# Optimization experiments

Measured on AMD Instinct MI355X. Metric: run time of the kernel, lower is better.

Reference implementation:

```python
import jax, jax.numpy as jnp
import numpy as np

D_MODEL = 512
N_EXPERTS = 8


def setup_inputs() -> dict:
    key = jax.random.key(0)
    ks = jax.random.split(key, 7)
    B, S, D, E = 8, 2048, D_MODEL, N_EXPERTS
    scale = 1.0 / np.sqrt(D)
    x = jax.random.normal(ks[0], (B, S, D), dtype=jnp.float32)
    W1 = jax.random.normal(ks[1], (E, D, D), dtype=jnp.float32) * scale
    b1 = jax.random.normal(ks[2], (E, D), dtype=jnp.float32) * scale
    W2 = jax.random.normal(ks[3], (E, D, D), dtype=jnp.float32) * scale
    b2 = jax.random.normal(ks[4], (E, D), dtype=jnp.float32) * scale
    Wg = jax.random.normal(ks[5], (D, E), dtype=jnp.float32) * scale
    bg = jax.random.normal(ks[6], (E,), dtype=jnp.float32) * scale
    return {"x": x, "W1": W1, "b1": b1, "W2": W2, "b2": b2, "Wg": Wg, "bg": bg}


def reference(x, W1, b1, W2, b2, Wg, bg):
    # All-experts dense MLP: h[e,b,s,f] = relu(x @ W1[e] + b1[e])
    h = jax.nn.relu(jnp.einsum('bsd,edf->ebsf', x, W1) + b1[:, None, None, :])
    expert_out = jnp.einsum('ebsf,efd->ebsd', h, W2) + b2[:, None, None, :]
    # Softmax gate over experts
    gates = jax.nn.softmax(jnp.einsum('bsd,de->bse', x, Wg) + bg, axis=-1)
    # Weighted combine: bsn, nbsd -> bsd
    return jnp.einsum('bsn,nbsd->bsd', gates, expert_out)
```

## Files before the change

### kernel.cpp

```cpp
#include <hip/hip_runtime.h>

typedef __attribute__((ext_vector_type(8))) short short8;
typedef __attribute__((ext_vector_type(4))) float f32x4;
typedef __attribute__((ext_vector_type(16))) float f32x16;

#define T_TOK 16384
#define DM 512
#define NE 8
#define BM 64
#define ROWB 1040

__device__ __forceinline__ ushort f2bf(float v) {
  unsigned u = __float_as_uint(v);
  return (ushort)((u + 0x7FFFu + ((u >> 16) & 1u)) >> 16);
}

__global__ void gates_kernel(const float* __restrict__ x, const float* __restrict__ Wg,
                             const float* __restrict__ bg, float* __restrict__ gates) {
  int wid = (int)((blockIdx.x * blockDim.x + threadIdx.x) >> 6);
  int lane = threadIdx.x & 63;
  if (wid >= T_TOK) return;
  const float* xt = x + (size_t)wid * DM;
  float a[NE];
#pragma unroll
  for (int e = 0; e < NE; ++e) a[e] = 0.f;
  for (int d = lane; d < DM; d += 64) {
    float xv = xt[d];
    const float* wr = Wg + d * NE;
#pragma unroll
    for (int e = 0; e < NE; ++e) a[e] += xv * wr[e];
  }
#pragma unroll
  for (int e = 0; e < NE; ++e) {
#pragma unroll
    for (int off = 32; off > 0; off >>= 1) a[e] += __shfl_xor(a[e], off, 64);
  }
  float m = -1e30f;
#pragma unroll
  for (int e = 0; e < NE; ++e) { a[e] += bg[e]; m = fmaxf(m, a[e]); }
  float s = 0.f;
#pragma unroll
  for (int e = 0; e < NE; ++e) { a[e] = __expf(a[e] - m); s += a[e]; }
  float inv = 1.f / s;
  if (lane < NE) gates[(size_t)wid * NE + lane] = a[lane] * inv;
}

__global__ void reorder_w_kernel(const float* __restrict__ W, ushort* __restrict__ WF) {
  int c = blockIdx.x * blockDim.x + threadIdx.x;
  int l = c & 63;
  int chunk = c >> 6;
  int ft = chunk & 15;
  int kh = (chunk >> 4) & 31;
  int e = chunk >> 9;
  int n = ft * 32 + (l & 31);
  int k0 = kh * 16 + (l >> 5) * 8;
  const float* src = W + ((size_t)e * DM + k0) * DM + n;
  short8 v;
#pragma unroll
  for (int j = 0; j < 8; ++j) v[j] = (short)f2bf(src[(size_t)j * DM]);
  *reinterpret_cast<short8*>(WF + (size_t)c * 8) = v;
}

__global__ __launch_bounds__(512, 2) void moe_main_kernel(
    const float* __restrict__ x, const ushort* __restrict__ W1F,
    const float* __restrict__ b1, const ushort* __restrict__ W2F,
    const float* __restrict__ b2, const float* __restrict__ gates,
    float* __restrict__ out) {
  extern __shared__ char smem[];
  char* x_lds = smem;
  char* h_lds = smem + 66560;
  float* g_lds = (float*)(smem + 133120);

  const int tid = threadIdx.x;
  const int lane = tid & 63;
  const int w = tid >> 6;
  const int hi = lane >> 5;
  const int l31 = lane & 31;
  const int m0 = blockIdx.x * BM;

  const unsigned abase = (unsigned)l31 * ROWB + (unsigned)hi * 16;
  const unsigned wbase = (unsigned)l31 * ROWB + (unsigned)(w * 128 + hi * 8);

#define BARRIER()                                        \
  do {                                                   \
    asm volatile("s_waitcnt lgkmcnt(0)" ::: "memory");   \
    __builtin_amdgcn_s_barrier();                        \
  } while (0)

  {
    int t = tid >> 3, e = tid & 7;
    g_lds[t * 9 + e] = gates[(size_t)(m0 + t) * NE + e];
  }

  for (int i = tid; i < BM * DM / 4; i += 512) {
    int t = i >> 7;
    int kd = (i & 127) * 4;
    float4 v = *reinterpret_cast<const float4*>(x + ((size_t)(m0 + t) << 9) + kd);
    unsigned lo = (unsigned)f2bf(v.x) | ((unsigned)f2bf(v.y) << 16);
    unsigned hb = (unsigned)f2bf(v.z) | ((unsigned)f2bf(v.w) << 16);
    *reinterpret_cast<uint2*>(x_lds + (unsigned)(t * ROWB + kd * 2)) = make_uint2(lo, hb);
  }
  BARRIER();

#define LDACT(lds, kt, ks, ni) \
  (*reinterpret_cast<const short8*>((lds) + abase + (ni) * (32 * ROWB) + ((kt) * 64 + (ks) * 32)))

#define MF(d, a, b) d = __builtin_amdgcn_mfma_f32_32x32x16_bf16(a, b, d, 0, 0, 0)

  const short8* wp1 = reinterpret_cast<const short8*>(W1F) + w * 128 + lane;
  const short8* wp2 = reinterpret_cast<const short8*>(W2F) + w * 128 + lane;

  f32x16 acc[2][2];
#pragma unroll
  for (int mi = 0; mi < 2; ++mi)
#pragma unroll
    for (int ni = 0; ni < 2; ++ni)
#pragma unroll
      for (int i = 0; i < 16; ++i) acc[mi][ni][i] = 0.f;

  short8 wb[3][4], ab[2][4];

#pragma unroll
  for (int ks = 0; ks < 2; ++ks)
#pragma unroll
    for (int mi = 0; mi < 2; ++mi) {
      wb[2][ks * 2 + mi] = wp1[ks * 1024 + mi * 64];
      wb[0][ks * 2 + mi] = wp1[2048 + ks * 1024 + mi * 64];
    }
#pragma unroll
  for (int ks = 0; ks < 2; ++ks)
#pragma unroll
    for (int ni = 0; ni < 2; ++ni) ab[0][ks * 2 + ni] = LDACT(x_lds, 0, ks, ni);

  for (int e = 0; e < NE; ++e) {
    const short8* we1 = wp1 + (size_t)e * 32768;
    const short8* we2 = wp2 + (size_t)e * 32768;

    f32x16 hacc[2][2];
#pragma unroll
    for (int mi = 0; mi < 2; ++mi)
#pragma unroll
      for (int ni = 0; ni < 2; ++ni)
#pragma unroll
        for (int i = 0; i < 16; ++i) hacc[mi][ni][i] = 0.f;

#pragma unroll
    for (int kt = 0; kt < 16; ++kt) {
      if (kt < 14) {
#pragma unroll
        for (int ks = 0; ks < 2; ++ks)
#pragma unroll
          for (int mi = 0; mi < 2; ++mi)
            wb[(kt + 1) % 3][ks * 2 + mi] = we1[(kt + 2) * 2048 + ks * 1024 + mi * 64];
      }
      if (kt < 15) {
#pragma unroll
        for (int ks = 0; ks < 2; ++ks)
#pragma unroll
          for (int ni = 0; ni < 2; ++ni)
            ab[(kt + 1) % 2][ks * 2 + ni] = LDACT(x_lds, kt + 1, ks, ni);
      }
      __builtin_amdgcn_s_setprio(1);
#pragma unroll
      for (int ks = 0; ks < 2; ++ks)
#pragma unroll
        for (int mi = 0; mi < 2; ++mi)
#pragma unroll
          for (int ni = 0; ni < 2; ++ni)
            MF(hacc[mi][ni], wb[(kt + 2) % 3][ks * 2 + mi], ab[kt % 2][ks * 2 + ni]);
      __builtin_amdgcn_s_setprio(0);
    }

#pragma unroll
    for (int ks = 0; ks < 2; ++ks)
#pragma unroll
      for (int mi = 0; mi < 2; ++mi) {
        wb[1][ks * 2 + mi] = we2[ks * 1024 + mi * 64];
        wb[2][ks * 2 + mi] = we2[2048 + ks * 1024 + mi * 64];
      }

#pragma unroll
    for (int ni = 0; ni < 2; ++ni) {
      int t = ni * 32 + l31;
      float g = g_lds[t * 9 + e];
#pragma unroll
      for (int mi = 0; mi < 2; ++mi) {
#pragma unroll
        for (int j = 0; j < 4; ++j) {
          float4 b1q = *reinterpret_cast<const float4*>(
              b1 + e * DM + w * 64 + mi * 32 + j * 8 + hi * 4);
          float v0 = fmaxf(hacc[mi][ni][j * 4 + 0] + b1q.x, 0.f) * g;
          float v1 = fmaxf(hacc[mi][ni][j * 4 + 1] + b1q.y, 0.f) * g;
          float v2 = fmaxf(hacc[mi][ni][j * 4 + 2] + b1q.z, 0.f) * g;
          float v3 = fmaxf(hacc[mi][ni][j * 4 + 3] + b1q.w, 0.f) * g;
          unsigned lo = (unsigned)f2bf(v0) | ((unsigned)f2bf(v1) << 16);
          unsigned hb = (unsigned)f2bf(v2) | ((unsigned)f2bf(v3) << 16);
          *reinterpret_cast<uint2*>(h_lds + wbase + ni * (32 * ROWB) + mi * 64 + j * 16) =
              make_uint2(lo, hb);
        }
      }
    }
    BARRIER();

#pragma unroll
    for (int ks = 0; ks < 2; ++ks)
#pragma unroll
      for (int ni = 0; ni < 2; ++ni) ab[0][ks * 2 + ni] = LDACT(h_lds, 0, ks, ni);

#pragma unroll
    for (int kt = 0; kt < 16; ++kt) {
      if (kt < 14) {
#pragma unroll
        for (int ks = 0; ks < 2; ++ks)
#pragma unroll
          for (int mi = 0; mi < 2; ++mi)
            wb[kt % 3][ks * 2 + mi] = we2[(kt + 2) * 2048 + ks * 1024 + mi * 64];
      }
      if (kt < 15) {
#pragma unroll
        for (int ks = 0; ks < 2; ++ks)
#pragma unroll
          for (int ni = 0; ni < 2; ++ni)
            ab[(kt + 1) % 2][ks * 2 + ni] = LDACT(h_lds, kt + 1, ks, ni);
      }
      __builtin_amdgcn_s_setprio(1);
#pragma unroll
      for (int ks = 0; ks < 2; ++ks)
#pragma unroll
        for (int mi = 0; mi < 2; ++mi)
#pragma unroll
          for (int ni = 0; ni < 2; ++ni)
            MF(acc[mi][ni], wb[(kt + 1) % 3][ks * 2 + mi], ab[kt % 2][ks * 2 + ni]);
      __builtin_amdgcn_s_setprio(0);
    }

    if (e < NE - 1) {
      const short8* wn1 = we1 + 32768;
#pragma unroll
      for (int ks = 0; ks < 2; ++ks)
#pragma unroll
        for (int mi = 0; mi < 2; ++mi) {
          wb[2][ks * 2 + mi] = wn1[ks * 1024 + mi * 64];
          wb[0][ks * 2 + mi] = wn1[2048 + ks * 1024 + mi * 64];
        }
#pragma unroll
      for (int ks = 0; ks < 2; ++ks)
#pragma unroll
        for (int ni = 0; ni < 2; ++ni) ab[0][ks * 2 + ni] = LDACT(x_lds, 0, ks, ni);
    }

#pragma unroll
    for (int ni = 0; ni < 2; ++ni) {
      int t = ni * 32 + l31;
      float g = g_lds[t * 9 + e];
#pragma unroll
      for (int mi = 0; mi < 2; ++mi)
#pragma unroll
        for (int j = 0; j < 4; ++j) {
          float4 b2q = *reinterpret_cast<const float4*>(
              b2 + e * DM + w * 64 + mi * 32 + j * 8 + hi * 4);
          acc[mi][ni][j * 4 + 0] += g * b2q.x;
          acc[mi][ni][j * 4 + 1] += g * b2q.y;
          acc[mi][ni][j * 4 + 2] += g * b2q.z;
          acc[mi][ni][j * 4 + 3] += g * b2q.w;
        }
    }
    BARRIER();
  }

#pragma unroll
  for (int ni = 0; ni < 2; ++ni) {
    int t = m0 + ni * 32 + l31;
#pragma unroll
    for (int mi = 0; mi < 2; ++mi)
#pragma unroll
      for (int j = 0; j < 4; ++j) {
        f32x4 v;
        v[0] = acc[mi][ni][j * 4 + 0];
        v[1] = acc[mi][ni][j * 4 + 1];
        v[2] = acc[mi][ni][j * 4 + 2];
        v[3] = acc[mi][ni][j * 4 + 3];
        *reinterpret_cast<f32x4*>(out + (size_t)t * DM + w * 64 + mi * 32 + j * 8 + hi * 4) = v;
      }
  }
#undef LDACT
#undef MF
#undef BARRIER
}

extern "C" void kernel_launch(void* const* d_in, const int* in_sizes, int n_in,
                              void* d_out, int out_size, void* d_ws, size_t ws_size,
                              hipStream_t stream) {
  const float* x  = (const float*)d_in[0];
  const float* W1 = (const float*)d_in[1];
  const float* b1 = (const float*)d_in[2];
  const float* W2 = (const float*)d_in[3];
  const float* b2 = (const float*)d_in[4];
  const float* Wg = (const float*)d_in[5];
  const float* bg = (const float*)d_in[6];
  float* out = (float*)d_out;

  float* gates = (float*)d_ws;
  ushort* W1F = (ushort*)((char*)d_ws + 524288);
  ushort* W2F = (ushort*)((char*)d_ws + 524288 + 4194304);

  hipFuncSetAttribute((const void*)moe_main_kernel,
                      hipFuncAttributeMaxDynamicSharedMemorySize, 135424);

  gates_kernel<<<T_TOK / 4, 256, 0, stream>>>(x, Wg, bg, gates);
  reorder_w_kernel<<<1024, 256, 0, stream>>>(W1, W1F);
  reorder_w_kernel<<<1024, 256, 0, stream>>>(W2, W2F);
  moe_main_kernel<<<T_TOK / BM, 512, 135424, stream>>>(x, W1F, b1, W2F, b2, gates, out);
}
```

Baseline: 167.8 us.

## Interleave next expert's first GEMM with current expert's second GEMM

The per-expert loop is software-pipelined across experts. The W1 GEMM for expert e+1 is computed inside the same k-loop as the W2 GEMM for expert e, so the MFMA chains of the two independent accumulators can hide each other's latency. A prologue handles expert 0's first GEMM and the last expert runs W2 alone. The b2 bias-times-gate accumulation moves out of the expert loop into a single epilogue. Weight prefetch drops from triple-buffered to double-buffered A/B register sets, and both accumulator sets stay live, which raises register pressure.

Result: slower. 308.2 us (+83.7%).

```diff
diff --git a/kernel.cpp b/kernel.cpp
--- a/kernel.cpp
+++ b/kernel.cpp
@@ -87,6 +87,11 @@
     __builtin_amdgcn_s_barrier();                        \
   } while (0)
 
+#define LDACT(lds, kt, ks, ni) \
+  (*reinterpret_cast<const short8*>((lds) + abase + (ni) * (32 * ROWB) + ((kt) * 64 + (ks) * 32)))
+
+#define MF(d, a, b) d = __builtin_amdgcn_mfma_f32_32x32x16_bf16(a, b, d, 0, 0, 0)
+
   {
     int t = tid >> 3, e = tid & 7;
     g_lds[t * 9 + e] = gates[(size_t)(m0 + t) * NE + e];
@@ -100,84 +105,70 @@
     unsigned hb = (unsigned)f2bf(v.z) | ((unsigned)f2bf(v.w) << 16);
     *reinterpret_cast<uint2*>(x_lds + (unsigned)(t * ROWB + kd * 2)) = make_uint2(lo, hb);
   }
-  BARRIER();
-
-#define LDACT(lds, kt, ks, ni) \
-  (*reinterpret_cast<const short8*>((lds) + abase + (ni) * (32 * ROWB) + ((kt) * 64 + (ks) * 32)))
-
-#define MF(d, a, b) d = __builtin_amdgcn_mfma_f32_32x32x16_bf16(a, b, d, 0, 0, 0)
 
   const short8* wp1 = reinterpret_cast<const short8*>(W1F) + w * 128 + lane;
   const short8* wp2 = reinterpret_cast<const short8*>(W2F) + w * 128 + lane;
 
   f32x16 acc[2][2];
+  f32x16 hacc[2][2];
 #pragma unroll
   for (int mi = 0; mi < 2; ++mi)
 #pragma unroll
     for (int ni = 0; ni < 2; ++ni)
 #pragma unroll
-      for (int i = 0; i < 16; ++i) acc[mi][ni][i] = 0.f;
-
-  short8 wb[3][4], ab[2][4];
+      for (int i = 0; i < 16; ++i) { acc[mi][ni][i] = 0.f; hacc[mi][ni][i] = 0.f; }
+
+  short8 wA[2][4];
+  short8 wB[2][4];
 
 #pragma unroll
   for (int ks = 0; ks < 2; ++ks)
 #pragma unroll
-    for (int mi = 0; mi < 2; ++mi) {
-      wb[2][ks * 2 + mi] = wp1[ks * 1024 + mi * 64];
-      wb[0][ks * 2 + mi] = wp1[2048 + ks * 1024 + mi * 64];
+    for (int mi = 0; mi < 2; ++mi) wB[0][ks * 2 + mi] = wp1[ks * 1024 + mi * 64];
+
+  BARRIER();
+
+#pragma unroll
+  for (int kt = 0; kt < 16; ++kt) {
+    if (kt < 15) {
+#pragma unroll
+      for (int ks = 0; ks < 2; ++ks)
+#pragma unroll
+        for (int mi = 0; mi < 2; ++mi)
+          wB[(kt + 1) & 1][ks * 2 + mi] = wp1[(kt + 1) * 2048 + ks * 1024 + mi * 64];
     }
-#pragma unroll
-  for (int ks = 0; ks < 2; ++ks)
-#pragma unroll
-    for (int ni = 0; ni < 2; ++ni) ab[0][ks * 2 + ni] = LDACT(x_lds, 0, ks, ni);
+    short8 a1[4];
+#pragma unroll
+    for (int ks = 0; ks < 2; ++ks)
+#pragma unroll
+      for (int ni = 0; ni < 2; ++ni) a1[ks * 2 + ni] = LDACT(x_lds, kt, ks, ni);
+    __builtin_amdgcn_s_setprio(1);
+#pragma unroll
+    for (int ks = 0; ks < 2; ++ks)
+#pragma unroll
+      for (int mi = 0; mi < 2; ++mi)
+#pragma unroll
+        for (int ni = 0; ni < 2; ++ni)
+          MF(hacc[mi][ni], wB[kt & 1][ks * 2 + mi], a1[ks * 2 + ni]);
+    __builtin_amdgcn_s_setprio(0);
+  }
 
   for (int e = 0; e < NE; ++e) {
-    const short8* we1 = wp1 + (size_t)e * 32768;
     const short8* we2 = wp2 + (size_t)e * 32768;
-
-    f32x16 hacc[2][2];
-#pragma unroll
-    for (int mi = 0; mi < 2; ++mi)
-#pragma unroll
-      for (int ni = 0; ni < 2; ++ni)
-#pragma unroll
-        for (int i = 0; i < 16; ++i) hacc[mi][ni][i] = 0.f;
-
-#pragma unroll
-    for (int kt = 0; kt < 16; ++kt) {
-      if (kt < 14) {
-#pragma unroll
-        for (int ks = 0; ks < 2; ++ks)
-#pragma unroll
-          for (int mi = 0; mi < 2; ++mi)
-            wb[(kt + 1) % 3][ks * 2 + mi] = we1[(kt + 2) * 2048 + ks * 1024 + mi * 64];
-      }
-      if (kt < 15) {
-#pragma unroll
-        for (int ks = 0; ks < 2; ++ks)
-#pragma unroll
-          for (int ni = 0; ni < 2; ++ni)
-            ab[(kt + 1) % 2][ks * 2 + ni] = LDACT(x_lds, kt + 1, ks, ni);
-      }
-      __builtin_amdgcn_s_setprio(1);
+    const short8* wn1 = wp1 + (size_t)(e + 1) * 32768;
+
+    BARRIER();
+
+#pragma unroll
+    for (int ks = 0; ks < 2; ++ks)
+#pragma unroll
+      for (int mi = 0; mi < 2; ++mi) wA[0][ks * 2 + mi] = we2[ks * 1024 + mi * 64];
+    if (e < NE - 1) {
 #pragma unroll
       for (int ks = 0; ks < 2; ++ks)
 #pragma unroll
-        for (int mi = 0; mi < 2; ++mi)
-#pragma unroll
-          for (int ni = 0; ni < 2; ++ni)
-            MF(hacc[mi][ni], wb[(kt + 2) % 3][ks * 2 + mi], ab[kt % 2][ks * 2 + ni]);
-      __builtin_amdgcn_s_setprio(0);
+        for (int mi = 0; mi < 2; ++mi) wB[0][ks * 2 + mi] = wn1[ks * 1024 + mi * 64];
     }
-
-#pragma unroll
-    for (int ks = 0; ks < 2; ++ks)
-#pragma unroll
-      for (int mi = 0; mi < 2; ++mi) {
-        wb[1][ks * 2 + mi] = we2[ks * 1024 + mi * 64];
-        wb[2][ks * 2 + mi] = we2[2048 + ks * 1024 + mi * 64];
-      }
 
 #pragma unroll
     for (int ni = 0; ni < 2; ++ni) {
@@ -202,70 +193,92 @@
     }
     BARRIER();
 
-#pragma unroll
-    for (int ks = 0; ks < 2; ++ks)
-#pragma unroll
-      for (int ni = 0; ni < 2; ++ni) ab[0][ks * 2 + ni] = LDACT(h_lds, 0, ks, ni);
-
-#pragma unroll
-    for (int kt = 0; kt < 16; ++kt) {
-      if (kt < 14) {
+    if (e < NE - 1) {
+#pragma unroll
+      for (int mi = 0; mi < 2; ++mi)
+#pragma unroll
+        for (int ni = 0; ni < 2; ++ni)
+#pragma unroll
+          for (int i = 0; i < 16; ++i) hacc[mi][ni][i] = 0.f;
+
+#pragma unroll
+      for (int kt = 0; kt < 16; ++kt) {
+        if (kt < 15) {
+#pragma unroll
+          for (int ks = 0; ks < 2; ++ks)
+#pragma unroll
+            for (int mi = 0; mi < 2; ++mi) {
+              wA[(kt + 1) & 1][ks * 2 + mi] = we2[(kt + 1) * 2048 + ks * 1024 + mi * 64];
+              wB[(kt + 1) & 1][ks * 2 + mi] = wn1[(kt + 1) * 2048 + ks * 1024 + mi * 64];
+            }
+        }
+        short8 a2[4], a1[4];
 #pragma unroll
         for (int ks = 0; ks < 2; ++ks)
 #pragma unroll
+          for (int ni = 0; ni < 2; ++ni) {
+            a2[ks * 2 + ni] = LDACT(h_lds, kt, ks, ni);
+            a1[ks * 2 + ni] = LDACT(x_lds, kt, ks, ni);
+          }
+        __builtin_amdgcn_s_setprio(1);
+#pragma unroll
+        for (int ks = 0; ks < 2; ++ks)
+#pragma unroll
           for (int mi = 0; mi < 2; ++mi)
-            wb[kt % 3][ks * 2 + mi] = we2[(kt + 2) * 2048 + ks * 1024 + mi * 64];
-      }
-      if (kt < 15) {
+#pragma unroll
+            for (int ni = 0; ni < 2; ++ni) {
+              MF(acc[mi][ni], wA[kt & 1][ks * 2 + mi], a2[ks * 2 + ni]);
+              MF(hacc[mi][ni], wB[kt & 1][ks * 2 + mi], a1[ks * 2 + ni]);
+            }
+        __builtin_amdgcn_s_setprio(0);
+      }
+    } else {
+#pragma unroll
+      for (int kt = 0; kt < 16; ++kt) {
+        if (kt < 15) {
+#pragma unroll
+          for (int ks = 0; ks < 2; ++ks)
+#pragma unroll
+            for (int mi = 0; mi < 2; ++mi)
+              wA[(kt + 1) & 1][ks * 2 + mi] = we2[(kt + 1) * 2048 + ks * 1024 + mi * 64];
+        }
+        short8 a2[4];
 #pragma unroll
         for (int ks = 0; ks < 2; ++ks)
 #pragma unroll
-          for (int ni = 0; ni < 2; ++ni)
-            ab[(kt + 1) % 2][ks * 2 + ni] = LDACT(h_lds, kt + 1, ks, ni);
-      }
-      __builtin_amdgcn_s_setprio(1);
-#pragma unroll
-      for (int ks = 0; ks < 2; ++ks)
-#pragma unroll
-        for (int mi = 0; mi < 2; ++mi)
-#pragma unroll
-          for (int ni = 0; ni < 2; ++ni)
-            MF(acc[mi][ni], wb[(kt + 1) % 3][ks * 2 + mi], ab[kt % 2][ks * 2 + ni]);
-      __builtin_amdgcn_s_setprio(0);
+          for (int ni = 0; ni < 2; ++ni) a2[ks * 2 + ni] = LDACT(h_lds, kt, ks, ni);
+        __builtin_amdgcn_s_setprio(1);
+#pragma unroll
+        for (int ks = 0; ks < 2; ++ks)
+#pragma unroll
+          for (int mi = 0; mi < 2; ++mi)
+#pragma unroll
+            for (int ni = 0; ni < 2; ++ni)
+              MF(acc[mi][ni], wA[kt & 1][ks * 2 + mi], a2[ks * 2 + ni]);
+        __builtin_amdgcn_s_setprio(0);
+      }
     }
-
-    if (e < NE - 1) {
-      const short8* wn1 = we1 + 32768;
-#pragma unroll
-      for (int ks = 0; ks < 2; ++ks)
-#pragma unroll
-        for (int mi = 0; mi < 2; ++mi) {
-          wb[2][ks * 2 + mi] = wn1[ks * 1024 + mi * 64];
-          wb[0][ks * 2 + mi] = wn1[2048 + ks * 1024 + mi * 64];
-        }
-#pragma unroll
-      for (int ks = 0; ks < 2; ++ks)
-#pragma unroll
-        for (int ni = 0; ni < 2; ++ni) ab[0][ks * 2 + ni] = LDACT(x_lds, 0, ks, ni);
-    }
-
-#pragma unroll
-    for (int ni = 0; ni < 2; ++ni) {
-      int t = ni * 32 + l31;
-      float g = g_lds[t * 9 + e];
-#pragma unroll
-      for (int mi = 0; mi < 2; ++mi)
-#pragma unroll
-        for (int j = 0; j < 4; ++j) {
-          float4 b2q = *reinterpret_cast<const float4*>(
-              b2 + e * DM + w * 64 + mi * 32 + j * 8 + hi * 4);
-          acc[mi][ni][j * 4 + 0] += g * b2q.x;
-          acc[mi][ni][j * 4 + 1] += g * b2q.y;
-          acc[mi][ni][j * 4 + 2] += g * b2q.z;
-          acc[mi][ni][j * 4 + 3] += g * b2q.w;
-        }
-    }
-    BARRIER();
+  }
+
+#pragma unroll
+  for (int e = 0; e < NE; ++e) {
+    float ge0 = g_lds[l31 * 9 + e];
+    float ge1 = g_lds[(32 + l31) * 9 + e];
+#pragma unroll
+    for (int mi = 0; mi < 2; ++mi)
+#pragma unroll
+      for (int j = 0; j < 4; ++j) {
+        float4 b2q = *reinterpret_cast<const float4*>(
+            b2 + e * DM + w * 64 + mi * 32 + j * 8 + hi * 4);
+        acc[mi][0][j * 4 + 0] += ge0 * b2q.x;
+        acc[mi][0][j * 4 + 1] += ge0 * b2q.y;
+        acc[mi][0][j * 4 + 2] += ge0 * b2q.z;
+        acc[mi][0][j * 4 + 3] += ge0 * b2q.w;
+        acc[mi][1][j * 4 + 0] += ge1 * b2q.x;
+        acc[mi][1][j * 4 + 1] += ge1 * b2q.y;
+        acc[mi][1][j * 4 + 2] += ge1 * b2q.z;
+        acc[mi][1][j * 4 + 3] += ge1 * b2q.w;
+      }
   }
 
 #pragma unroll
```
